# Performance work log

Hardware: AMD Instinct MI355X
Metric: run time of the kernel (lower is better)

The kernel has to match this reference:

```python
import jax, jax.numpy as jnp
import numpy as np

NEG_INF = -1e9  # finite large-negative for the additive causal mask
N, H, S, SKV, K, V = 4, 16, 2048, 2048, 128, 128


def setup_inputs() -> dict:
    key = jax.random.key(0)
    k1, k2, k3, k4 = jax.random.split(key, 4)
    seqs = jax.random.normal(k1, (N, H, S, K), dtype=jnp.float32)
    keys = jax.random.normal(k2, (N, H, SKV, K), dtype=jnp.float32)
    values = jax.random.normal(k3, (N, H, SKV, V), dtype=jnp.float32)
    # boolean keep-mask; force first key position valid so no row is fully masked
    kpm = jax.random.randint(k4, (N, SKV), 0, 2) > 0
    kpm = kpm.at[:, 0].set(True)
    # causal additive attention mask, shape (S, S_kv)
    causal = jnp.tril(jnp.ones((S, SKV), dtype=bool))
    attn_mask = jnp.where(causal, 0.0, NEG_INF).astype(jnp.float32)
    return {"seqs": seqs, "keys": keys, "values": values,
            "key_padding_mask": kpm, "attn_mask": attn_mask}


def reference(seqs, keys, values, key_padding_mask, attn_mask):
    # attn_weights: [N,H,S,S_kv]
    scale = seqs.shape[-1] ** -0.5
    w = jnp.einsum('bhsk,bhtk->bhst', seqs, keys) * scale
    w = w + attn_mask  # broadcast (S,S_kv) over (N,H)
    w = jnp.where(key_padding_mask[:, None, None, :], w, -jnp.inf)
    # softmax computed in fp32, then cast back to input dtype (matches torch)
    p = jax.nn.softmax(w.astype(jnp.float32), axis=-1).astype(seqs.dtype)
    attn = jnp.einsum('bhst,bhtv->bhsv', p, values)
    return attn
```

## Files before the change

### kernel.cpp

```cpp
#include <hip/hip_runtime.h>

#define S_Q 2048
#define S_KV 2048
#define D_K 128
#define NH 64
#define QSCALE 0.12751494907890272f

typedef __attribute__((ext_vector_type(8))) short s16x8;
typedef __attribute__((ext_vector_type(16))) float f32x16;

__device__ __attribute__((aligned(16))) unsigned short g_Kb[(size_t)NH * S_KV * D_K];
__device__ __attribute__((aligned(16))) unsigned short g_Vt[(size_t)NH * D_K * S_KV];

__device__ inline unsigned short f2bf(float f) {
  unsigned int u = __float_as_uint(f);
  u += 0x7FFFu + ((u >> 16) & 1u);
  return (unsigned short)(u >> 16);
}

__device__ inline void plane32_swap(unsigned& a, unsigned& b) {
#if __has_builtin(__builtin_amdgcn_permlane32_swap)
  typedef unsigned __attribute__((ext_vector_type(2))) u32x2;
  u32x2 r = __builtin_amdgcn_permlane32_swap(a, b, false, false);
  a = r.x; b = r.y;
#else
  asm volatile("v_permlane32_swap_b32 %0, %1" : "+v"(a), "+v"(b));
#endif
}

__global__ __launch_bounds__(256) void prep_k_kernel(const float* __restrict__ K) {
  size_t g = (size_t)blockIdx.x * 256 + threadIdx.x;
  const float* src = K + g * 8;
  float4 x = *(const float4*)src;
  float4 y = *(const float4*)(src + 4);
  union { uint4 q; unsigned short u[8]; } t;
  t.u[0] = f2bf(x.x); t.u[1] = f2bf(x.y); t.u[2] = f2bf(x.z); t.u[3] = f2bf(x.w);
  t.u[4] = f2bf(y.x); t.u[5] = f2bf(y.y); t.u[6] = f2bf(y.z); t.u[7] = f2bf(y.w);
  ((uint4*)g_Kb)[g] = t.q;
}

__global__ __launch_bounds__(256) void prep_v_kernel(const float* __restrict__ V) {
  __shared__ float tile_f[64][33];
  int bid = blockIdx.x;
  int bh = bid >> 7;
  int rem = bid & 127;
  int t0 = (rem >> 2) << 6;
  int v0 = (rem & 3) << 5;
  int c = threadIdx.x & 31;
  int r8 = threadIdx.x >> 5;
#pragma unroll
  for (int i = 0; i < 8; i++) {
    int r = r8 + i * 8;
    tile_f[r][c] = V[((size_t)(bh * S_KV + t0 + r)) * D_K + v0 + c];
  }
  __syncthreads();
  int vv = threadIdx.x >> 3;
  int jc = threadIdx.x & 7;
  union { uint4 q; unsigned short u[8]; } t;
#pragma unroll
  for (int u8 = 0; u8 < 8; u8++) t.u[u8] = f2bf(tile_f[jc * 8 + u8][vv]);
  *(uint4*)&g_Vt[((size_t)(bh * D_K + v0 + vv)) * S_KV + t0 + jc * 8] = t.q;
}

__global__ __launch_bounds__(256, 2) void attn_kernel(const float* __restrict__ Q,
                                                      const int* __restrict__ kpm,
                                                      float* __restrict__ out) {
  __shared__ unsigned short sK[2][32 * 136];
  __shared__ unsigned short sV[2][128 * 40];
  __shared__ unsigned sMask[64];

  const int bx = blockIdx.x;
  const int bh = ((bx & 7) << 3) | ((bx >> 3) & 7);
  int qp = bx >> 6;
  int qi = (qp & 4) ? ((qp & 8) ? qp - 8 : qp - 4) : ((qp & 8) ? 19 - qp : 15 - qp);
  const int q0 = qi << 7;
  const int tid = threadIdx.x;
  const int w = tid >> 6;
  const int ln = tid & 31;
  const int h = (tid >> 5) & 1;
  const int h8 = h * 8;
  const int qw = q0 + w * 32;
  const int qln = qw + ln;
  const int b = bh >> 4;

  {
    int base = w * 512;
#pragma unroll
    for (int rr = 0; rr < 8; rr++) {
      int idx = base + rr * 64 + (tid & 63);
      unsigned long long bal = __ballot(kpm[b * S_KV + idx] != 0);
      if ((tid & 63) == 0) {
        sMask[(base >> 5) + rr * 2] = (unsigned)bal;
        sMask[(base >> 5) + rr * 2 + 1] = (unsigned)(bal >> 32);
      }
    }
  }

  s16x8 qf[8];
  {
    const float* qrow = Q + ((size_t)(bh * S_Q + qln)) * D_K + h8;
#pragma unroll
    for (int kc = 0; kc < 8; kc++) {
      float4 x = *(const float4*)(qrow + kc * 16);
      float4 y = *(const float4*)(qrow + kc * 16 + 4);
      union { s16x8 v; unsigned short u[8]; } t;
      t.u[0] = f2bf(x.x * QSCALE); t.u[1] = f2bf(x.y * QSCALE);
      t.u[2] = f2bf(x.z * QSCALE); t.u[3] = f2bf(x.w * QSCALE);
      t.u[4] = f2bf(y.x * QSCALE); t.u[5] = f2bf(y.y * QSCALE);
      t.u[6] = f2bf(y.z * QSCALE); t.u[7] = f2bf(y.w * QSCALE);
      qf[kc] = t.v;
    }
  }

  const int id0 = tid, id1 = 256 + tid;
  const int kr0r = id0 >> 4, kr0c = (id0 & 15) * 8;
  const int kr1r = id1 >> 4, kr1c = (id1 & 15) * 8;
  const int vr0r = id0 >> 2, vr0c = (id0 & 3) * 8;
  const int vr1r = id1 >> 2, vr1c = (id1 & 3) * 8;
  uint4 rk0, rk1, rv0, rv1;
  auto load_tile = [&](int t0) {
    rk0 = *(const uint4*)&g_Kb[((size_t)(bh * S_KV + t0 + kr0r)) * D_K + kr0c];
    rk1 = *(const uint4*)&g_Kb[((size_t)(bh * S_KV + t0 + kr1r)) * D_K + kr1c];
    rv0 = *(const uint4*)&g_Vt[((size_t)(bh * D_K + vr0r)) * S_KV + t0 + vr0c];
    rv1 = *(const uint4*)&g_Vt[((size_t)(bh * D_K + vr1r)) * S_KV + t0 + vr1c];
  };
  auto store_tile = [&](int buf) {
    *(uint4*)&sK[buf][kr0r * 136 + kr0c] = rk0;
    *(uint4*)&sK[buf][kr1r * 136 + kr1c] = rk1;
    *(uint4*)&sV[buf][vr0r * 40 + vr0c] = rv0;
    *(uint4*)&sV[buf][vr1r * 40 + vr1c] = rv1;
  };

  f32x16 o[4] = {f32x16{}, f32x16{}, f32x16{}, f32x16{}};
  float lsum = 0.0f;

  const int nT = qi * 4 + 4;
  load_tile(0);
  store_tile(0);
  load_tile(32);
  __syncthreads();

  for (int i = 0; i < nT; i++) {
    const int cur = i & 1;
    if (i + 1 < nT) {
      store_tile(1 - cur);
      if (i + 2 < nT) load_tile((i + 2) * 32);
    }
    const int t0 = i * 32;
    if (t0 <= qw + 31) {
      const unsigned km = sMask[i];
      f32x16 sa = {};
#pragma unroll
      for (int kc = 0; kc < 8; kc++) {
        s16x8 kb = *(const s16x8*)&sK[cur][ln * 136 + kc * 16 + h8];
        sa = __builtin_amdgcn_mfma_f32_32x32x16_bf16(kb, qf[kc], sa, 0, 0, 0);
      }
      int thr = qln - t0;
      unsigned causal = (thr >= 31) ? 0xFFFFFFFFu : ((thr < 0) ? 0u : ((2u << thr) - 1u));
      unsigned pmh = (km & causal) >> (h * 4);
      float p[16];
#pragma unroll
      for (int r = 0; r < 16; r++) {
        const int tb = (r & 3) + 8 * (r >> 2);
        float e = __builtin_amdgcn_exp2f(sa[r]);
        float bitf = (float)((pmh >> tb) & 1u);
        p[r] = e * bitf;
        lsum += p[r];
      }
      unsigned d[8];
#pragma unroll
      for (int m = 0; m < 4; m++) {
        d[2 * m] = __builtin_amdgcn_perm(__float_as_uint(p[4 * m + 1]),
                                         __float_as_uint(p[4 * m + 0]), 0x07060302u);
        d[2 * m + 1] = __builtin_amdgcn_perm(__float_as_uint(p[4 * m + 3]),
                                             __float_as_uint(p[4 * m + 2]), 0x07060302u);
      }
      plane32_swap(d[0], d[2]); plane32_swap(d[1], d[3]);
      plane32_swap(d[4], d[6]); plane32_swap(d[5], d[7]);
      union { unsigned u[4]; s16x8 v; } pu0, pu1;
      pu0.u[0] = d[0]; pu0.u[1] = d[1]; pu0.u[2] = d[2]; pu0.u[3] = d[3];
      pu1.u[0] = d[4]; pu1.u[1] = d[5]; pu1.u[2] = d[6]; pu1.u[3] = d[7];
#pragma unroll
      for (int vt = 0; vt < 4; vt++) {
        s16x8 va = *(const s16x8*)&sV[cur][(vt * 32 + ln) * 40 + h8];
        s16x8 vb = *(const s16x8*)&sV[cur][(vt * 32 + ln) * 40 + 16 + h8];
        o[vt] = __builtin_amdgcn_mfma_f32_32x32x16_bf16(va, pu0.v, o[vt], 0, 0, 0);
        o[vt] = __builtin_amdgcn_mfma_f32_32x32x16_bf16(vb, pu1.v, o[vt], 0, 0, 0);
      }
    }
    __syncthreads();
  }

  float ltot = lsum + __shfl_xor(lsum, 32, 64);
  float invl = 1.0f / ltot;
  size_t orow = ((size_t)(bh * S_Q + qln)) * D_K;
#pragma unroll
  for (int vt = 0; vt < 4; vt++) {
#pragma unroll
    for (int qd = 0; qd < 4; qd++) {
      float4 vv;
      vv.x = o[vt][4 * qd + 0] * invl;
      vv.y = o[vt][4 * qd + 1] * invl;
      vv.z = o[vt][4 * qd + 2] * invl;
      vv.w = o[vt][4 * qd + 3] * invl;
      *(float4*)&out[orow + vt * 32 + qd * 8 + 4 * h] = vv;
    }
  }
}

extern "C" void kernel_launch(void* const* d_in, const int* in_sizes, int n_in,
                              void* d_out, int out_size, void* d_ws, size_t ws_size,
                              hipStream_t stream) {
  const float* Q = (const float*)d_in[0];
  const float* K = (const float*)d_in[1];
  const float* V = (const float*)d_in[2];
  const int* kpm = (const int*)d_in[3];
  float* out = (float*)d_out;
  hipLaunchKernelGGL(prep_k_kernel, dim3(8192), dim3(256), 0, stream, K);
  hipLaunchKernelGGL(prep_v_kernel, dim3(8192), dim3(256), 0, stream, V);
  hipLaunchKernelGGL(attn_kernel, dim3(1024), dim3(256), 0, stream, Q, kpm, out);
}
```

Baseline: 323.3 us.

## Merge prep kernels, pre-zero masked V, raise occupancy, and reorder tile stores

Merges the K and V bf16 conversion kernels into one launch. The V prep now zeroes rows whose key-padding mask is off. The attention kernel asks for 3 blocks per CU instead of 2. It uses v_cvt_pk_bf16_f32 for the P packing (round-to-nearest instead of truncation) and replaces the float-multiply mask with a select. The next-tile LDS store moves after the compute, with a custom waitcnt plus barrier, and the causal skip condition is tightened to t0 <= qw. Together these aim to cut launch overhead and per-tile ALU work and to improve latency hiding, at the cost of register pressure from the higher occupancy target.

```diff
diff --git a/kernel.cpp b/kernel.cpp
--- a/kernel.cpp
+++ b/kernel.cpp
@@ -4,6 +4,7 @@
 #define S_KV 2048
 #define D_K 128
 #define NH 64
+#define NB 4
 #define QSCALE 0.12751494907890272f
 
 typedef __attribute__((ext_vector_type(8))) short s16x8;
@@ -16,6 +17,12 @@
   unsigned int u = __float_as_uint(f);
   u += 0x7FFFu + ((u >> 16) & 1u);
   return (unsigned short)(u >> 16);
+}
+
+__device__ inline unsigned cvt_pk_bf16(float lo, float hi) {
+  unsigned r;
+  asm("v_cvt_pk_bf16_f32 %0, %1, %2" : "=v"(r) : "v"(lo), "v"(hi));
+  return r;
 }
 
 __device__ inline void plane32_swap(unsigned& a, unsigned& b) {
@@ -28,45 +35,50 @@
 #endif
 }
 
-__global__ __launch_bounds__(256) void prep_k_kernel(const float* __restrict__ K) {
-  size_t g = (size_t)blockIdx.x * 256 + threadIdx.x;
-  const float* src = K + g * 8;
-  float4 x = *(const float4*)src;
-  float4 y = *(const float4*)(src + 4);
-  union { uint4 q; unsigned short u[8]; } t;
-  t.u[0] = f2bf(x.x); t.u[1] = f2bf(x.y); t.u[2] = f2bf(x.z); t.u[3] = f2bf(x.w);
-  t.u[4] = f2bf(y.x); t.u[5] = f2bf(y.y); t.u[6] = f2bf(y.z); t.u[7] = f2bf(y.w);
-  ((uint4*)g_Kb)[g] = t.q;
-}
-
-__global__ __launch_bounds__(256) void prep_v_kernel(const float* __restrict__ V) {
+__global__ __launch_bounds__(256) void prep_kernel(const float* __restrict__ K,
+                                                   const float* __restrict__ V,
+                                                   const int* __restrict__ kpm) {
   __shared__ float tile_f[64][33];
-  int bid = blockIdx.x;
-  int bh = bid >> 7;
-  int rem = bid & 127;
-  int t0 = (rem >> 2) << 6;
-  int v0 = (rem & 3) << 5;
-  int c = threadIdx.x & 31;
-  int r8 = threadIdx.x >> 5;
-#pragma unroll
-  for (int i = 0; i < 8; i++) {
-    int r = r8 + i * 8;
-    tile_f[r][c] = V[((size_t)(bh * S_KV + t0 + r)) * D_K + v0 + c];
-  }
-  __syncthreads();
-  int vv = threadIdx.x >> 3;
-  int jc = threadIdx.x & 7;
-  union { uint4 q; unsigned short u[8]; } t;
-#pragma unroll
-  for (int u8 = 0; u8 < 8; u8++) t.u[u8] = f2bf(tile_f[jc * 8 + u8][vv]);
-  *(uint4*)&g_Vt[((size_t)(bh * D_K + v0 + vv)) * S_KV + t0 + jc * 8] = t.q;
-}
-
-__global__ __launch_bounds__(256, 2) void attn_kernel(const float* __restrict__ Q,
+  const int bid = blockIdx.x;
+  if (bid < 8192) {
+    size_t g = (size_t)bid * 256 + threadIdx.x;
+    const float* src = K + g * 8;
+    float4 x = *(const float4*)src;
+    float4 y = *(const float4*)(src + 4);
+    union { uint4 q; unsigned short u[8]; } t;
+    t.u[0] = f2bf(x.x); t.u[1] = f2bf(x.y); t.u[2] = f2bf(x.z); t.u[3] = f2bf(x.w);
+    t.u[4] = f2bf(y.x); t.u[5] = f2bf(y.y); t.u[6] = f2bf(y.z); t.u[7] = f2bf(y.w);
+    ((uint4*)g_Kb)[g] = t.q;
+  } else {
+    const int vb = bid - 8192;
+    int bh = vb >> 7;
+    int rem = vb & 127;
+    int t0 = (rem >> 2) << 6;
+    int v0 = (rem & 3) << 5;
+    int c = threadIdx.x & 31;
+    int r8 = threadIdx.x >> 5;
+    const int* kp = kpm + (bh >> 4) * S_KV + t0;
+#pragma unroll
+    for (int i = 0; i < 8; i++) {
+      int r = r8 + i * 8;
+      float f = V[((size_t)(bh * S_KV + t0 + r)) * D_K + v0 + c];
+      tile_f[r][c] = kp[r] ? f : 0.0f;
+    }
+    __syncthreads();
+    int vv = threadIdx.x >> 3;
+    int jc = threadIdx.x & 7;
+    union { uint4 q; unsigned short u[8]; } t;
+#pragma unroll
+    for (int u8 = 0; u8 < 8; u8++) t.u[u8] = f2bf(tile_f[jc * 8 + u8][vv]);
+    *(uint4*)&g_Vt[((size_t)(bh * D_K + v0 + vv)) * S_KV + t0 + jc * 8] = t.q;
+  }
+}
+
+__global__ __launch_bounds__(256, 3) void attn_kernel(const float* __restrict__ Q,
                                                       const int* __restrict__ kpm,
                                                       float* __restrict__ out) {
-  __shared__ unsigned short sK[2][32 * 136];
-  __shared__ unsigned short sV[2][128 * 40];
+  __shared__ __attribute__((aligned(16))) unsigned short sK[2][32 * 136];
+  __shared__ __attribute__((aligned(16))) unsigned short sV[2][128 * 40];
   __shared__ unsigned sMask[64];
 
   const int bx = blockIdx.x;
@@ -137,24 +149,20 @@
   const int nT = qi * 4 + 4;
   load_tile(0);
   store_tile(0);
+  __syncthreads();
   load_tile(32);
-  __syncthreads();
 
   for (int i = 0; i < nT; i++) {
     const int cur = i & 1;
-    if (i + 1 < nT) {
-      store_tile(1 - cur);
-      if (i + 2 < nT) load_tile((i + 2) * 32);
-    }
     const int t0 = i * 32;
-    if (t0 <= qw + 31) {
-      const unsigned km = sMask[i];
+    if (t0 <= qw) {
       f32x16 sa = {};
 #pragma unroll
       for (int kc = 0; kc < 8; kc++) {
         s16x8 kb = *(const s16x8*)&sK[cur][ln * 136 + kc * 16 + h8];
         sa = __builtin_amdgcn_mfma_f32_32x32x16_bf16(kb, qf[kc], sa, 0, 0, 0);
       }
+      const unsigned km = sMask[i];
       int thr = qln - t0;
       unsigned causal = (thr >= 31) ? 0xFFFFFFFFu : ((thr < 0) ? 0u : ((2u << thr) - 1u));
       unsigned pmh = (km & causal) >> (h * 4);
@@ -163,17 +171,14 @@
       for (int r = 0; r < 16; r++) {
         const int tb = (r & 3) + 8 * (r >> 2);
         float e = __builtin_amdgcn_exp2f(sa[r]);
-        float bitf = (float)((pmh >> tb) & 1u);
-        p[r] = e * bitf;
+        p[r] = ((pmh >> tb) & 1u) ? e : 0.0f;
         lsum += p[r];
       }
       unsigned d[8];
 #pragma unroll
       for (int m = 0; m < 4; m++) {
-        d[2 * m] = __builtin_amdgcn_perm(__float_as_uint(p[4 * m + 1]),
-                                         __float_as_uint(p[4 * m + 0]), 0x07060302u);
-        d[2 * m + 1] = __builtin_amdgcn_perm(__float_as_uint(p[4 * m + 3]),
-                                             __float_as_uint(p[4 * m + 2]), 0x07060302u);
+        d[2 * m] = cvt_pk_bf16(p[4 * m + 0], p[4 * m + 1]);
+        d[2 * m + 1] = cvt_pk_bf16(p[4 * m + 2], p[4 * m + 3]);
       }
       plane32_swap(d[0], d[2]); plane32_swap(d[1], d[3]);
       plane32_swap(d[4], d[6]); plane32_swap(d[5], d[7]);
@@ -188,7 +193,13 @@
         o[vt] = __builtin_amdgcn_mfma_f32_32x32x16_bf16(vb, pu1.v, o[vt], 0, 0, 0);
       }
     }
-    __syncthreads();
+    if (i + 1 < nT) {
+      store_tile(1 - cur);
+      if (i + 2 < nT) load_tile((i + 2) * 32);
+    }
+    __builtin_amdgcn_sched_barrier(0);
+    asm volatile("s_waitcnt lgkmcnt(0)" ::: "memory");
+    __builtin_amdgcn_s_barrier();
   }
 
   float ltot = lsum + __shfl_xor(lsum, 32, 64);
@@ -216,7 +227,6 @@
   const float* V = (const float*)d_in[2];
   const int* kpm = (const int*)d_in[3];
   float* out = (float*)d_out;
-  hipLaunchKernelGGL(prep_k_kernel, dim3(8192), dim3(256), 0, stream, K);
-  hipLaunchKernelGGL(prep_v_kernel, dim3(8192), dim3(256), 0, stream, V);
+  hipLaunchKernelGGL(prep_kernel, dim3(16384), dim3(256), 0, stream, K, V, kpm);
   hipLaunchKernelGGL(attn_kernel, dim3(1024), dim3(256), 0, stream, Q, kpm, out);
 }
```

After: 306.6 us. -5.1%, faster.
